# Kernel tuning notes

Measured on AMD Instinct MI355X. Metric: run time of the kernel, lower is better.

## Reference

```python
import jax, jax.numpy as jnp
import numpy as np

B = 64            # number of graphs
N = 2048          # nodes per graph (equal segments; torch.stack in the original requires this)
D = 256           # hidden_dim
G = 4             # num_groups
SUBS = 3          # subclasses per group -> num_classes = 12
C = G * SUBS


def _layer_norm(x, g, b, eps=1e-5):
    mu = jnp.mean(x, axis=-1, keepdims=True)
    var = jnp.var(x, axis=-1, keepdims=True)
    return (x - mu) * jax.lax.rsqrt(var + eps) * g + b


def setup_inputs() -> dict:
    key = jax.random.key(0)
    ks = jax.random.split(key, 20)
    T = B * N
    inp = {
        "node_features": jax.random.normal(ks[0], (T, D), dtype=jnp.float32),
        "batch": jnp.repeat(jnp.arange(B, dtype=jnp.int64), N),  # sorted, equal-size segments
        # group queries (nn.Parameter randn)
        "group_queries": jax.random.normal(ks[1], (G, D), dtype=jnp.float32),
        # per-group projector MLP: D -> 2D -> SUBS*D (stacked over groups)
        "proj_w1": jax.random.normal(ks[2], (G, D, 2 * D), dtype=jnp.float32) * (1.0 / np.sqrt(D)),
        "proj_b1": jnp.zeros((G, 2 * D), dtype=jnp.float32),
        "proj_w2": jax.random.normal(ks[3], (G, 2 * D, SUBS * D), dtype=jnp.float32) * (1.0 / np.sqrt(2 * D)),
        "proj_b2": jnp.zeros((G, SUBS * D), dtype=jnp.float32),
        # output_proj_12: LN -> Linear(D, D//2) -> ReLU -> Linear(D//2, 1)
        "ln12_g": jnp.ones((D,), dtype=jnp.float32),
        "ln12_b": jnp.zeros((D,), dtype=jnp.float32),
        "w12a": jax.random.normal(ks[4], (D, D // 2), dtype=jnp.float32) * (1.0 / np.sqrt(D)),
        "b12a": jnp.zeros((D // 2,), dtype=jnp.float32),
        "w12b": jax.random.normal(ks[5], (D // 2, 1), dtype=jnp.float32) * (1.0 / np.sqrt(D // 2)),
        "b12b": jnp.zeros((1,), dtype=jnp.float32),
        # output_proj_4
        "ln4_g": jnp.ones((D,), dtype=jnp.float32),
        "ln4_b": jnp.zeros((D,), dtype=jnp.float32),
        "w4a": jax.random.normal(ks[6], (D, D // 2), dtype=jnp.float32) * (1.0 / np.sqrt(D)),
        "b4a": jnp.zeros((D // 2,), dtype=jnp.float32),
        "w4b": jax.random.normal(ks[7], (D // 2, 1), dtype=jnp.float32) * (1.0 / np.sqrt(D // 2)),
        "b4b": jnp.zeros((1,), dtype=jnp.float32),
    }
    return inp


def reference(node_features, batch, group_queries, proj_w1, proj_b1, proj_w2, proj_b2,
              ln12_g, ln12_b, w12a, b12a, w12b, b12b,
              ln4_g, ln4_b, w4a, b4a, w4b, b4b):
    # --- derive class queries from group queries (per-group MLP) ---
    h = jax.nn.relu(jnp.einsum('gd,gdh->gh', group_queries, proj_w1) + proj_b1)   # [G, 2D]
    flat = jnp.einsum('gh,ghk->gk', h, proj_w2) + proj_b2                         # [G, SUBS*D]
    # group g maps to global class indices [3g, 3g+1, 3g+2] -> simple reshape gives ordered queries
    class_queries = flat.reshape(C, D)                                            # [12, D]

    scale = jnp.asarray(D ** 0.5, node_features.dtype)
    # equal-size sorted segments: reshape total nodes into [B, N, D] per-graph blocks
    nodes = node_features.reshape(B, N, D)

    # --- 12-class attention pooling ---
    scores12 = jnp.einsum('cd,bnd->bcn', class_queries, nodes) / scale            # [B, 12, N]
    attn12 = jax.nn.softmax(scores12, axis=-1)
    pooled12 = jnp.einsum('bcn,bnd->bcd', attn12, nodes)                          # [B, 12, D]
    x12 = _layer_norm(pooled12, ln12_g, ln12_b)
    logits_12 = (jax.nn.relu(x12 @ w12a + b12a) @ w12b + b12b)[..., 0]            # [B, 12]

    # --- 4-group attention pooling ---
    scores4 = jnp.einsum('gd,bnd->bgn', group_queries, nodes) / scale             # [B, 4, N]
    attn4 = jax.nn.softmax(scores4, axis=-1)
    pooled4 = jnp.einsum('bgn,bnd->bgd', attn4, nodes)                            # [B, 4, D]
    x4 = _layer_norm(pooled4, ln4_g, ln4_b)
    logits_4 = (jax.nn.relu(x4 @ w4a + b4a) @ w4b + b4b)[..., 0]                  # [B, 4]

    return (logits_12, logits_4, attn12)
```

## Files before the change

### kernel.cpp

```cpp
#include <hip/hip_runtime.h>
#include <math.h>

#define BG   64
#define NN   2048
#define DD   256
#define CQ   16
#define CN   128
#define NCH  16

static constexpr size_t WS_Q16 = 0;
static constexpr size_t WS_H   = 4096;
static constexpr size_t WS_S   = 6144;
static constexpr size_t WS_ML  = WS_S + (size_t)BG * CQ * NN;
static constexpr size_t WS_PL  = WS_ML + (size_t)BG * NCH * 32;

__global__ __launch_bounds__(256) void kA1(const float* __restrict__ gq,
                                           const float* __restrict__ w1,
                                           const float* __restrict__ b1,
                                           float* __restrict__ ws) {
    int blk = blockIdx.x;
    int g   = blk >> 4;
    int jb  = (blk & 15) * 32;
    int t   = threadIdx.x;
    __shared__ float qlds[256];
    qlds[t] = gq[g * 256 + t];
    if ((blk & 15) == 0) ws[WS_Q16 + (12 + g) * 256 + t] = gq[g * 256 + t];
    __syncthreads();
    int jl = t & 31, dp = t >> 5;
    float acc = 0.f;
    const float* wp = w1 + ((size_t)g * 256) * 512 + jb + jl;
    #pragma unroll 8
    for (int i = 0; i < 32; ++i) {
        int d = dp * 32 + i;
        acc += qlds[d] * wp[(size_t)d * 512];
    }
    __shared__ float red[8][33];
    red[dp][jl] = acc;
    __syncthreads();
    if (dp == 0) {
        float s = 0.f;
        #pragma unroll
        for (int p = 0; p < 8; ++p) s += red[p][jl];
        s += b1[g * 512 + jb + jl];
        ws[WS_H + g * 512 + jb + jl] = fmaxf(s, 0.f);
    }
}

__global__ __launch_bounds__(256) void kA2(const float* __restrict__ w2,
                                           const float* __restrict__ b2,
                                           float* __restrict__ ws) {
    int blk = blockIdx.x;
    int g   = blk / 48;
    int kb  = (blk % 48) * 16;
    int t   = threadIdx.x;
    __shared__ float hlds[512];
    hlds[t]       = ws[WS_H + g * 512 + t];
    hlds[t + 256] = ws[WS_H + g * 512 + t + 256];
    __syncthreads();
    int kl = t & 15, dp = t >> 4;
    float acc = 0.f;
    const float* wp = w2 + ((size_t)g * 512) * 768 + kb + kl;
    #pragma unroll 8
    for (int i = 0; i < 32; ++i) {
        int jj = dp * 32 + i;
        acc += hlds[jj] * wp[(size_t)jj * 768];
    }
    __shared__ float red[16][17];
    red[dp][kl] = acc;
    __syncthreads();
    if (dp == 0) {
        float s = 0.f;
        #pragma unroll
        for (int p = 0; p < 16; ++p) s += red[p][kl];
        ws[WS_Q16 + g * 768 + kb + kl] = s + b2[g * 768 + kb + kl];
    }
}

__global__ __launch_bounds__(256) void kF(const float* __restrict__ x,
                                          float* __restrict__ ws) {
    __shared__ float4 qlds[CQ * 64];
    __shared__ float  wlds[CQ * CN];
    __shared__ float  mbuf[CQ], lbuf[CQ];

    int t   = threadIdx.x;
    int blk = blockIdx.x;
    int b   = blk >> 4, ch = blk & 15;
    int gn0 = b * NN + ch * CN;

    const float4* qg = (const float4*)(ws + WS_Q16);
    #pragma unroll
    for (int i = 0; i < 4; ++i) qlds[t + i * 256] = qg[t + i * 256];
    __syncthreads();

    int nl = t & 127, half = t >> 7;
    const float4* xa = (const float4*)x + (size_t)(gn0 + nl) * 64 + half * 32;
    float sc[CQ];
    #pragma unroll
    for (int c = 0; c < CQ; ++c) sc[c] = 0.f;

    float4 buf[8];
    #pragma unroll
    for (int i = 0; i < 8; ++i) buf[i] = xa[i];
    for (int base = 0; base < 32; base += 8) {
        float4 cur[8];
        #pragma unroll
        for (int i = 0; i < 8; ++i) cur[i] = buf[i];
        if (base + 8 < 32) {
            #pragma unroll
            for (int i = 0; i < 8; ++i) buf[i] = xa[base + 8 + i];
        }
        #pragma unroll
        for (int i = 0; i < 8; ++i) {
            #pragma unroll
            for (int c = 0; c < CQ; ++c) {
                float4 q = qlds[c * 64 + half * 32 + base + i];
                sc[c] += q.x * cur[i].x + q.y * cur[i].y
                       + q.z * cur[i].z + q.w * cur[i].w;
            }
        }
    }
    if (half == 1) {
        #pragma unroll
        for (int c = 0; c < CQ; ++c) wlds[c * CN + nl] = sc[c];
    }
    __syncthreads();
    if (half == 0) {
        float* srow = ws + WS_S + ((size_t)b * CQ) * NN + ch * CN;
        #pragma unroll
        for (int c = 0; c < CQ; ++c) {
            float full = (sc[c] + wlds[c * CN + nl]) * 0.0625f;
            srow[(size_t)c * NN + nl] = full;
            wlds[c * CN + nl] = full;
        }
    }
    __syncthreads();

    {
        int c = t >> 4, slot = t & 15;
        float mv = -1e30f;
        #pragma unroll
        for (int k = 0; k < 8; ++k) mv = fmaxf(mv, wlds[c * CN + slot + k * 16]);
        #pragma unroll
        for (int off = 8; off; off >>= 1) mv = fmaxf(mv, __shfl_xor(mv, off, 16));
        if (slot == 0) mbuf[c] = mv;
    }
    __syncthreads();
    {
        int c = t >> 4, slot = t & 15;
        float m = mbuf[c];
        float lv = 0.f;
        #pragma unroll
        for (int k = 0; k < 8; ++k) {
            float e = __expf(wlds[c * CN + slot + k * 16] - m);
            wlds[c * CN + slot + k * 16] = e;
            lv += e;
        }
        #pragma unroll
        for (int off = 8; off; off >>= 1) lv += __shfl_xor(lv, off, 16);
        if (slot == 0) lbuf[c] = lv;
    }
    __syncthreads();
    if (t < CQ) {
        ws[WS_ML + (size_t)blk * 32 + t]      = mbuf[t];
        ws[WS_ML + (size_t)blk * 32 + 16 + t] = lbuf[t];
    }

    int wave = t >> 6, lane = t & 63;
    float4 acc[CQ];
    #pragma unroll
    for (int c = 0; c < CQ; ++c) acc[c] = make_float4(0.f, 0.f, 0.f, 0.f);

    const float4* xq = (const float4*)x + (size_t)(gn0 + wave * 32) * 64 + lane;
    for (int nq = 0; nq < 8; ++nq) {
        float4 x0 = xq[(size_t)(nq * 4 + 0) * 64];
        float4 x1 = xq[(size_t)(nq * 4 + 1) * 64];
        float4 x2 = xq[(size_t)(nq * 4 + 2) * 64];
        float4 x3 = xq[(size_t)(nq * 4 + 3) * 64];
        #pragma unroll
        for (int c = 0; c < CQ; ++c) {
            float4 ev = *(const float4*)&wlds[c * CN + wave * 32 + nq * 4];
            acc[c].x += ev.x * x0.x + ev.y * x1.x + ev.z * x2.x + ev.w * x3.x;
            acc[c].y += ev.x * x0.y + ev.y * x1.y + ev.z * x2.y + ev.w * x3.y;
            acc[c].z += ev.x * x0.z + ev.y * x1.z + ev.z * x2.z + ev.w * x3.z;
            acc[c].w += ev.x * x0.w + ev.y * x1.w + ev.z * x2.w + ev.w * x3.w;
        }
    }

    float* sdata = (float*)qlds;
    for (int w = 0; w < 4; ++w) {
        if (wave == w) {
            #pragma unroll
            for (int c = 0; c < CQ; ++c) {
                float* dst = &sdata[c * 256 + lane * 4];
                if (w == 0) {
                    dst[0] = acc[c].x; dst[1] = acc[c].y;
                    dst[2] = acc[c].z; dst[3] = acc[c].w;
                } else {
                    dst[0] += acc[c].x; dst[1] += acc[c].y;
                    dst[2] += acc[c].z; dst[3] += acc[c].w;
                }
            }
        }
        __syncthreads();
    }
    float* po = ws + WS_PL + (size_t)blk * (CQ * 256);
    #pragma unroll
    for (int i = 0; i < CQ; ++i) po[t + i * 256] = sdata[t + i * 256];
}

__global__ __launch_bounds__(256) void kE(float* __restrict__ ws,
        const float* __restrict__ lnG12, const float* __restrict__ lnB12,
        const float* __restrict__ wA12,  const float* __restrict__ bA12,
        const float* __restrict__ wB12,  const float* __restrict__ bB12,
        const float* __restrict__ lnG4,  const float* __restrict__ lnB4,
        const float* __restrict__ wA4,   const float* __restrict__ bA4,
        const float* __restrict__ wB4,   const float* __restrict__ bB4,
        float* __restrict__ out, float* __restrict__ out_attn) {
    int bc = blockIdx.x;
    int b = bc >> 4, c = bc & 15;
    int t = threadIdx.x, wave = t >> 6, lane = t & 63;

    __shared__ float scl[NCH];
    __shared__ float smm, sil;
    if (t < NCH) {
        float mi = ws[WS_ML + (size_t)(b * NCH + t) * 32 + c];
        float li = ws[WS_ML + (size_t)(b * NCH + t) * 32 + 16 + c];
        float m = mi;
        #pragma unroll
        for (int off = 8; off; off >>= 1) m = fmaxf(m, __shfl_xor(m, off, 16));
        float sc = __expf(mi - m);
        float ls = sc * li;
        #pragma unroll
        for (int off = 8; off; off >>= 1) ls += __shfl_xor(ls, off, 16);
        scl[t] = sc;
        if (t == 0) { smm = m; sil = 1.f / ls; }
    }
    __syncthreads();
    float il = sil;

    float v = 0.f;
    #pragma unroll 4
    for (int i = 0; i < NCH; ++i)
        v += scl[i] * ws[WS_PL + ((size_t)(b * NCH + i) * CQ + c) * 256 + t];
    v *= il;

    __shared__ float wr1[4], wr2[4];
    float s = v;
    #pragma unroll
    for (int off = 32; off; off >>= 1) s += __shfl_xor(s, off, 64);
    if (lane == 0) wr1[wave] = s;
    __syncthreads();
    float mu = (wr1[0] + wr1[1] + wr1[2] + wr1[3]) * (1.f / 256.f);
    float dv = v - mu;
    s = dv * dv;
    #pragma unroll
    for (int off = 32; off; off >>= 1) s += __shfl_xor(s, off, 64);
    if (lane == 0) wr2[wave] = s;
    __syncthreads();
    float var = (wr2[0] + wr2[1] + wr2[2] + wr2[3]) * (1.f / 256.f);

    bool is12 = (c < 12);
    const float* lg = is12 ? lnG12 : lnG4;
    const float* lb = is12 ? lnB12 : lnB4;
    const float* wA = is12 ? wA12  : wA4;
    const float* bA = is12 ? bA12  : bA4;
    const float* wB = is12 ? wB12  : wB4;
    const float* bB = is12 ? bB12  : bB4;

    __shared__ float ylds[256];
    __shared__ float hred[256];
    __shared__ float hlds[128];
    float y = dv * rsqrtf(var + 1e-5f) * lg[t] + lb[t];
    ylds[t] = y;
    __syncthreads();
    {
        int j = t & 127, half = t >> 7;
        float hh = 0.f;
        const float* wc = wA + (size_t)half * 128 * 128 + j;
        #pragma unroll 4
        for (int d = 0; d < 128; ++d) hh += ylds[half * 128 + d] * wc[(size_t)d * 128];
        hred[t] = hh;
    }
    __syncthreads();
    if (t < 128) hlds[t] = fmaxf(hred[t] + hred[t + 128] + bA[t], 0.f);
    __syncthreads();
    if (t < 64) {
        float pp = hlds[t] * wB[t] + hlds[t + 64] * wB[t + 64];
        #pragma unroll
        for (int off = 32; off; off >>= 1) pp += __shfl_xor(pp, off, 64);
        if (t == 0) {
            float logit = pp + bB[0];
            if (is12) out[b * 12 + c] = logit;
            else      out[768 + b * 4 + (c - 12)] = logit;
        }
    }

    if (is12) {
        float m = smm;
        const float4* sr = (const float4*)(ws + WS_S + ((size_t)b * CQ + c) * NN);
        float4* ar = (float4*)out_attn + (size_t)(b * 12 + c) * (NN / 4);
        #pragma unroll
        for (int k = 0; k < 2; ++k) {
            float4 vv = sr[t + k * 256];
            float4 e;
            e.x = __expf(vv.x - m) * il;
            e.y = __expf(vv.y - m) * il;
            e.z = __expf(vv.z - m) * il;
            e.w = __expf(vv.w - m) * il;
            ar[t + k * 256] = e;
        }
    }
}

extern "C" void kernel_launch(void* const* d_in, const int* in_sizes, int n_in,
                              void* d_out, int out_size, void* d_ws, size_t ws_size,
                              hipStream_t stream) {
    const float* x     = (const float*)d_in[0];
    const float* gq    = (const float*)d_in[2];
    const float* w1    = (const float*)d_in[3];
    const float* b1    = (const float*)d_in[4];
    const float* w2    = (const float*)d_in[5];
    const float* b2    = (const float*)d_in[6];
    const float* ln12g = (const float*)d_in[7];
    const float* ln12b = (const float*)d_in[8];
    const float* w12a  = (const float*)d_in[9];
    const float* b12a  = (const float*)d_in[10];
    const float* w12b  = (const float*)d_in[11];
    const float* b12b  = (const float*)d_in[12];
    const float* ln4g  = (const float*)d_in[13];
    const float* ln4b  = (const float*)d_in[14];
    const float* w4a   = (const float*)d_in[15];
    const float* b4a   = (const float*)d_in[16];
    const float* w4b   = (const float*)d_in[17];
    const float* b4b   = (const float*)d_in[18];

    float* out = (float*)d_out;
    float* ws  = (float*)d_ws;

    kA1<<<64,       256, 0, stream>>>(gq, w1, b1, ws);
    kA2<<<192,      256, 0, stream>>>(w2, b2, ws);
    kF <<<BG * NCH, 256, 0, stream>>>(x, ws);
    kE <<<1024,     256, 0, stream>>>(ws,
            ln12g, ln12b, w12a, b12a, w12b, b12b,
            ln4g,  ln4b,  w4a,  b4a,  w4b,  b4b, out, out + 1024);
}
```

Measured before the change: 292.8 us.

## Widen fused scoring kernel to 512 threads with quad-split dot products

The fused score/softmax/pooling kernel now launches 512 threads per block instead of 256. In the scoring phase each group of four threads splits a node's 256-dim dot product and combines the partial sums with warp shuffles, replacing the two-half split that went through LDS and an extra barrier. In the pooling phase each of the eight waves handles 16 nodes instead of 32. The aim is more parallelism and latency hiding on the memory-bound node reads. The cost is a longer eight-step serialized cross-wave reduction, an extra barrier, and tighter register limits from the launch bound.

```diff
diff --git a/kernel.cpp b/kernel.cpp
--- a/kernel.cpp
+++ b/kernel.cpp
@@ -76,8 +76,8 @@
     }
 }
 
-__global__ __launch_bounds__(256) void kF(const float* __restrict__ x,
-                                          float* __restrict__ ws) {
+__global__ __launch_bounds__(512, 4) void kF(const float* __restrict__ x,
+                                             float* __restrict__ ws) {
     __shared__ float4 qlds[CQ * 64];
     __shared__ float  wlds[CQ * CN];
     __shared__ float  mbuf[CQ], lbuf[CQ];
@@ -88,54 +88,39 @@
     int gn0 = b * NN + ch * CN;
 
     const float4* qg = (const float4*)(ws + WS_Q16);
-    #pragma unroll
-    for (int i = 0; i < 4; ++i) qlds[t + i * 256] = qg[t + i * 256];
-    __syncthreads();
-
-    int nl = t & 127, half = t >> 7;
-    const float4* xa = (const float4*)x + (size_t)(gn0 + nl) * 64 + half * 32;
+    for (int i = t; i < CQ * 64; i += 512) qlds[i] = qg[i];
+    __syncthreads();
+
+    int qd = t & 3, nl = t >> 2;
+    const float4* xa = (const float4*)x + (size_t)(gn0 + nl) * 64 + qd * 16;
+    float4 xv[16];
+    #pragma unroll
+    for (int i = 0; i < 16; ++i) xv[i] = xa[i];
+
     float sc[CQ];
     #pragma unroll
-    for (int c = 0; c < CQ; ++c) sc[c] = 0.f;
-
-    float4 buf[8];
-    #pragma unroll
-    for (int i = 0; i < 8; ++i) buf[i] = xa[i];
-    for (int base = 0; base < 32; base += 8) {
-        float4 cur[8];
-        #pragma unroll
-        for (int i = 0; i < 8; ++i) cur[i] = buf[i];
-        if (base + 8 < 32) {
-            #pragma unroll
-            for (int i = 0; i < 8; ++i) buf[i] = xa[base + 8 + i];
-        }
-        #pragma unroll
-        for (int i = 0; i < 8; ++i) {
-            #pragma unroll
-            for (int c = 0; c < CQ; ++c) {
-                float4 q = qlds[c * 64 + half * 32 + base + i];
-                sc[c] += q.x * cur[i].x + q.y * cur[i].y
-                       + q.z * cur[i].z + q.w * cur[i].w;
-            }
-        }
-    }
-    if (half == 1) {
-        #pragma unroll
-        for (int c = 0; c < CQ; ++c) wlds[c * CN + nl] = sc[c];
-    }
-    __syncthreads();
-    if (half == 0) {
+    for (int c = 0; c < CQ; ++c) {
+        float a = 0.f;
+        #pragma unroll
+        for (int i = 0; i < 16; ++i) {
+            float4 q = qlds[c * 64 + qd * 16 + i];
+            a += q.x * xv[i].x + q.y * xv[i].y + q.z * xv[i].z + q.w * xv[i].w;
+        }
+        a += __shfl_xor(a, 1, 64);
+        a += __shfl_xor(a, 2, 64);
+        sc[c] = a * 0.0625f;
+    }
+    if (qd == 0) {
         float* srow = ws + WS_S + ((size_t)b * CQ) * NN + ch * CN;
         #pragma unroll
         for (int c = 0; c < CQ; ++c) {
-            float full = (sc[c] + wlds[c * CN + nl]) * 0.0625f;
-            srow[(size_t)c * NN + nl] = full;
-            wlds[c * CN + nl] = full;
-        }
-    }
-    __syncthreads();
-
-    {
+            srow[(size_t)c * NN + nl] = sc[c];
+            wlds[c * CN + nl] = sc[c];
+        }
+    }
+    __syncthreads();
+
+    if (t < 256) {
         int c = t >> 4, slot = t & 15;
         float mv = -1e30f;
         #pragma unroll
@@ -145,7 +130,7 @@
         if (slot == 0) mbuf[c] = mv;
     }
     __syncthreads();
-    {
+    if (t < 256) {
         int c = t >> 4, slot = t & 15;
         float m = mbuf[c];
         float lv = 0.f;
@@ -170,15 +155,16 @@
     #pragma unroll
     for (int c = 0; c < CQ; ++c) acc[c] = make_float4(0.f, 0.f, 0.f, 0.f);
 
-    const float4* xq = (const float4*)x + (size_t)(gn0 + wave * 32) * 64 + lane;
-    for (int nq = 0; nq < 8; ++nq) {
+    const float4* xq = (const float4*)x + (size_t)(gn0 + wave * 16) * 64 + lane;
+    #pragma unroll
+    for (int nq = 0; nq < 4; ++nq) {
         float4 x0 = xq[(size_t)(nq * 4 + 0) * 64];
         float4 x1 = xq[(size_t)(nq * 4 + 1) * 64];
         float4 x2 = xq[(size_t)(nq * 4 + 2) * 64];
         float4 x3 = xq[(size_t)(nq * 4 + 3) * 64];
         #pragma unroll
         for (int c = 0; c < CQ; ++c) {
-            float4 ev = *(const float4*)&wlds[c * CN + wave * 32 + nq * 4];
+            float4 ev = *(const float4*)&wlds[c * CN + wave * 16 + nq * 4];
             acc[c].x += ev.x * x0.x + ev.y * x1.x + ev.z * x2.x + ev.w * x3.x;
             acc[c].y += ev.x * x0.y + ev.y * x1.y + ev.z * x2.y + ev.w * x3.y;
             acc[c].z += ev.x * x0.z + ev.y * x1.z + ev.z * x2.z + ev.w * x3.z;
@@ -187,7 +173,8 @@
     }
 
     float* sdata = (float*)qlds;
-    for (int w = 0; w < 4; ++w) {
+    __syncthreads();
+    for (int w = 0; w < 8; ++w) {
         if (wave == w) {
             #pragma unroll
             for (int c = 0; c < CQ; ++c) {
@@ -205,7 +192,7 @@
     }
     float* po = ws + WS_PL + (size_t)blk * (CQ * 256);
     #pragma unroll
-    for (int i = 0; i < CQ; ++i) po[t + i * 256] = sdata[t + i * 256];
+    for (int i = 0; i < 8; ++i) po[t + i * 512] = sdata[t + i * 512];
 }
 
 __global__ __launch_bounds__(256) void kE(float* __restrict__ ws,
@@ -339,7 +326,7 @@
 
     kA1<<<64,       256, 0, stream>>>(gq, w1, b1, ws);
     kA2<<<192,      256, 0, stream>>>(w2, b2, ws);
-    kF <<<BG * NCH, 256, 0, stream>>>(x, ws);
+    kF <<<BG * NCH, 512, 0, stream>>>(x, ws);
     kE <<<1024,     256, 0, stream>>>(ws,
             ln12g, ln12b, w12a, b12a, w12b, b12b,
             ln4g,  ln4b,  w4a,  b4a,  w4b,  b4b, out, out + 1024);
```

Measured after the change: 309.0 us. 5.5% more time.
